# Kernel tuning notes

Measured on AMD Instinct MI355X. Metric: run time of the kernel, lower is better.

## Reference

```python
import jax, jax.numpy as jnp
import numpy as np

B, T, D, H = 8, 4096, 1024, 8
BW = D // H
MIN_DECAY = 0.001
EPS = 1e-05        # RGLRU eps (clamps)
SCAN_EPS = 1e-07   # closed_form_rnn_scan eps


def setup_inputs() -> dict:
    key = jax.random.key(0)
    k0, k1, k2 = jax.random.split(key, 3)
    x = jax.random.normal(k0, (B, T, D), dtype=jnp.float32)
    a_param = jnp.full((D,), -3.0, dtype=jnp.float32)
    # block-diagonal gate params (orthogonal-ish init approximated by scaled normal)
    w_in = jax.random.normal(k1, (H, BW, BW), dtype=jnp.float32) * (1.0 / np.sqrt(BW))
    b_in = jnp.ones((H, BW), dtype=jnp.float32)
    w_a = jax.random.normal(k2, (H, BW, BW), dtype=jnp.float32) * (1.0 / np.sqrt(BW))
    b_a = jnp.ones((H, BW), dtype=jnp.float32)
    return {"x": x, "a_param": a_param, "w_in": w_in, "b_in": b_in, "w_a": w_a, "b_a": b_a}


def block_diag_linear(x, w, b):
    # x: [B,T,D] -> [B,T,H,BW] ; w: [H,BW,BW] ; b: [H,BW]
    xb = x.reshape(x.shape[:-1] + (H, BW))
    y = jnp.einsum('bthi,hij->bthj', xb, w) + b
    return y.reshape(x.shape)


def closed_form_rnn_scan(x, a):
    # x, a: [B,T,D]; h0 = 0
    a_cumprod = jnp.cumprod(a, axis=1)
    ones = jnp.ones((x.shape[0], 1, x.shape[2]), dtype=x.dtype)
    p_prefix = jnp.concatenate([ones, a_cumprod[:, :-1, :]], axis=1)
    p_prefix = jnp.maximum(p_prefix, SCAN_EPS)
    w = (x + SCAN_EPS) / p_prefix
    S = jnp.cumsum(w, axis=1)
    h = p_prefix * S  # + p_prefix * h0 with h0 = 0
    return h, h[:, -1, :]


def reference(x, a_param, w_in, b_in, w_a, b_a):
    gate_x = jax.nn.sigmoid(block_diag_linear(x, w_in, b_in))
    gate_a = jax.nn.sigmoid(block_diag_linear(x, w_a, b_a))
    log_a = -gate_a * (jax.nn.softplus(a_param) + MIN_DECAY)
    a = jnp.minimum(jnp.exp(log_a), 1.0 - EPS)
    gated_x = x * gate_x
    multiplier = jnp.sqrt(jnp.maximum(1.0 - a * a, EPS))
    normed_x = gated_x * multiplier
    h, _ = closed_form_rnn_scan(normed_x, a)
    return h
```

## Files before the change

### kernel.cpp

```cpp
#include <hip/hip_runtime.h>

#define B_ 8
#define T_ 4096
#define D_ 1024
#define H_ 8
#define BW_ 128
#define NC_ 32
#define CT_ 128
#define EPS7 1e-7f
#define EPS5 1e-5f
#define LOG1MEPS -1.0000186e-05f

typedef _Float16 f16x8 __attribute__((ext_vector_type(8)));
typedef _Float16 f16x4 __attribute__((ext_vector_type(4)));
typedef float f32x4 __attribute__((ext_vector_type(4)));

__global__ __launch_bounds__(256) void k1_gates(
    const float* __restrict__ x, const float* __restrict__ a_param,
    const float* __restrict__ w_in, const float* __restrict__ b_in,
    const float* __restrict__ w_a, const float* __restrict__ b_a,
    float* __restrict__ Abuf, float* __restrict__ NX, float* __restrict__ CS)
{
  const int bid  = blockIdx.x;
  const int kc   = bid & (NC_ - 1);
  const int h    = (bid >> 5) & (H_ - 1);
  const int b    = bid >> 8;
  const int tid  = threadIdx.x;
  const int wave = tid >> 6;
  const int lane = tid & 63;
  const int quad = lane >> 4;
  const int l15  = lane & 15;

  __shared__ _Float16 xs[128 * 136];

  const float* xg = x + (size_t)(b * T_ + kc * CT_) * D_ + h * BW_;
  const int jc = wave * 32;

  f16x8 bf[2][2][4];
  #pragma unroll
  for (int g = 0; g < 2; ++g) {
    const float* wptr = (g ? w_a : w_in) + h * BW_ * BW_;
    #pragma unroll
    for (int jt = 0; jt < 2; ++jt) {
      #pragma unroll
      for (int k = 0; k < 4; ++k) {
        const float* wp = wptr + (k * 32 + quad * 8) * BW_ + jc + jt * 16 + l15;
        f16x8 f;
        #pragma unroll
        for (int i = 0; i < 8; ++i) f[i] = (_Float16)wp[i * BW_];
        bf[g][jt][k] = f;
      }
    }
  }
  float bI[2], bA[2], cdec[2];
  #pragma unroll
  for (int jt = 0; jt < 2; ++jt) {
    const int j = h * BW_ + jc + jt * 16 + l15;
    bI[jt] = b_in[j];
    bA[jt] = b_a[j];
    const float ap = a_param[j];
    cdec[jt] = ((ap > 20.f) ? ap : log1pf(__expf(ap))) + 0.001f;
  }

  {
    const int row = tid >> 1;
    const int cb  = (tid & 1) * 64;
    #pragma unroll
    for (int i = 0; i < 16; ++i) {
      const float4 v = *(const float4*)(xg + row * D_ + cb + i * 4);
      f16x4 hv = { (_Float16)v.x, (_Float16)v.y, (_Float16)v.z, (_Float16)v.w };
      *(f16x4*)(xs + row * 136 + cb + i * 4) = hv;
    }
  }
  __syncthreads();

  f32x4 acc[2][2][8];
  #pragma unroll
  for (int g = 0; g < 2; ++g)
    #pragma unroll
    for (int jt = 0; jt < 2; ++jt)
      #pragma unroll
      for (int m = 0; m < 8; ++m)
        acc[g][jt][m] = (f32x4){0.f, 0.f, 0.f, 0.f};

  #pragma unroll
  for (int m = 0; m < 8; ++m) {
    f16x8 af[4];
    #pragma unroll
    for (int k = 0; k < 4; ++k)
      af[k] = *(const f16x8*)(xs + (m * 16 + l15) * 136 + k * 32 + quad * 8);
    #pragma unroll
    for (int k = 0; k < 4; ++k)
      #pragma unroll
      for (int g = 0; g < 2; ++g)
        #pragma unroll
        for (int jt = 0; jt < 2; ++jt)
          acc[g][jt][m] = __builtin_amdgcn_mfma_f32_16x16x32_f16(
              af[k], bf[g][jt][k], acc[g][jt][m], 0, 0, 0);
  }

  float sla[2] = {0.f, 0.f};
  const size_t obase = (size_t)(b * T_ + kc * CT_) * D_ + h * BW_;
  #pragma unroll
  for (int m = 0; m < 8; ++m) {
    #pragma unroll
    for (int r = 0; r < 4; ++r) {
      const int row = m * 16 + quad * 4 + r;
      #pragma unroll
      for (int jt = 0; jt < 2; ++jt) {
        const int col = jc + jt * 16 + l15;
        const float yi = acc[0][jt][m][r] + bI[jt];
        const float ya = acc[1][jt][m][r] + bA[jt];
        const float gx = __builtin_amdgcn_rcpf(1.f + __expf(-yi));
        const float ga = __builtin_amdgcn_rcpf(1.f + __expf(-ya));
        const float la = -ga * cdec[jt];
        const float a  = fminf(__expf(la), 1.0f - EPS5);
        const float mult = sqrtf(fmaxf(fmaf(-a, a, 1.0f), EPS5));
        const float xval = xg[row * D_ + col];
        const float nx = xval * gx * mult;
        const size_t gi = obase + (size_t)row * D_ + col;
        Abuf[gi] = a;
        NX[gi]   = nx;
        sla[jt] += fminf(la, LOG1MEPS);
      }
    }
  }
  #pragma unroll
  for (int jt = 0; jt < 2; ++jt) {
    sla[jt] += __shfl_xor(sla[jt], 16, 64);
    sla[jt] += __shfl_xor(sla[jt], 32, 64);
  }
  if (quad == 0) {
    const int cs = (b * NC_ + kc) * D_ + h * BW_ + jc;
    CS[cs + l15]      = sla[0];
    CS[cs + 16 + l15] = sla[1];
  }
}

__global__ __launch_bounds__(256) void k2_scan_logs(float* __restrict__ CS)
{
  const int idx = blockIdx.x * 256 + threadIdx.x;
  const int b = idx >> 10;
  const int d = idx & (D_ - 1);
  float lq = 0.f;
  #pragma unroll
  for (int kk = 0; kk < NC_; ++kk) {
    const int o = (b * NC_ + kk) * D_ + d;
    const float c = CS[o];
    CS[o] = lq;
    lq += c;
  }
}

__device__ __forceinline__ float scan_r(float c, float pp, float aprev) {
  return (c > EPS7) ? aprev
                    : ((pp > EPS7) ? (EPS7 * __builtin_amdgcn_rcpf(pp)) : 1.0f);
}

__global__ __launch_bounds__(256) void k3_summary(
    const float* __restrict__ Abuf, const float* __restrict__ NX,
    const float* __restrict__ LQ, float* __restrict__ Ak, float* __restrict__ Bk)
{
  const int bid = blockIdx.x;
  const int g = bid & 3;
  const int k = (bid >> 2) & (NC_ - 1);
  const int b = bid >> 7;
  const int d = g * 256 + threadIdx.x;
  const int t0 = k * CT_;
  const size_t base = (size_t)(b * T_ + t0) * D_ + d;

  float c, pp, aprev;
  if (k == 0) { c = 1.f; pp = 1.f; aprev = 1.f; }
  else {
    c = __expf(LQ[(b * NC_ + k) * D_ + d]);
    aprev = Abuf[base - D_];
    pp = fmaxf(c / aprev, EPS7);
  }
  float hv = 0.f, rp = 1.f;
  for (int t = 0; t < CT_; t += 8) {
    float av[8], uv[8];
    #pragma unroll
    for (int i = 0; i < 8; ++i) {
      av[i] = Abuf[base + (size_t)(t + i) * D_];
      uv[i] = NX[base + (size_t)(t + i) * D_] + EPS7;
    }
    #pragma unroll
    for (int i = 0; i < 8; ++i) {
      const float p = fmaxf(c, EPS7);
      const float r = scan_r(c, pp, aprev);
      hv = fmaf(r, hv, uv[i]);
      rp *= r;
      c *= av[i]; pp = p; aprev = av[i];
    }
  }
  Ak[(b * NC_ + k) * D_ + d] = rp;
  Bk[(b * NC_ + k) * D_ + d] = hv;
}

__global__ __launch_bounds__(256) void k3_carry(
    float* __restrict__ Ak, const float* __restrict__ Bk)
{
  const int idx = blockIdx.x * 256 + threadIdx.x;
  const int b = idx >> 10;
  const int d = idx & (D_ - 1);
  float Hv = 0.f;
  #pragma unroll
  for (int kk = 0; kk < NC_; ++kk) {
    const int o = (b * NC_ + kk) * D_ + d;
    const float Av = Ak[o];
    Ak[o] = Hv;
    Hv = fmaf(Av, Hv, Bk[o]);
  }
}

__global__ __launch_bounds__(256) void k3_scan(
    const float* __restrict__ Abuf, float* NXO,
    const float* __restrict__ LQ, const float* __restrict__ Hc)
{
  const int bid = blockIdx.x;
  const int g = bid & 3;
  const int k = (bid >> 2) & (NC_ - 1);
  const int b = bid >> 7;
  const int d = g * 256 + threadIdx.x;
  const int t0 = k * CT_;
  const size_t base = (size_t)(b * T_ + t0) * D_ + d;

  float c, pp, aprev;
  if (k == 0) { c = 1.f; pp = 1.f; aprev = 1.f; }
  else {
    c = __expf(LQ[(b * NC_ + k) * D_ + d]);
    aprev = Abuf[base - D_];
    pp = fmaxf(c / aprev, EPS7);
  }
  float hv = Hc[(b * NC_ + k) * D_ + d];
  for (int t = 0; t < CT_; t += 8) {
    float av[8], uv[8];
    #pragma unroll
    for (int i = 0; i < 8; ++i) {
      av[i] = Abuf[base + (size_t)(t + i) * D_];
      uv[i] = NXO[base + (size_t)(t + i) * D_] + EPS7;
    }
    #pragma unroll
    for (int i = 0; i < 8; ++i) {
      const float p = fmaxf(c, EPS7);
      const float r = scan_r(c, pp, aprev);
      hv = fmaf(r, hv, uv[i]);
      NXO[base + (size_t)(t + i) * D_] = hv;
      c *= av[i]; pp = p; aprev = av[i];
    }
  }
}

extern "C" void kernel_launch(void* const* d_in, const int* in_sizes, int n_in,
                              void* d_out, int out_size, void* d_ws, size_t ws_size,
                              hipStream_t stream) {
  const float* x       = (const float*)d_in[0];
  const float* a_param = (const float*)d_in[1];
  const float* w_in    = (const float*)d_in[2];
  const float* b_in    = (const float*)d_in[3];
  const float* w_a     = (const float*)d_in[4];
  const float* b_a     = (const float*)d_in[5];
  float* out = (float*)d_out;

  char* ws = (char*)d_ws;
  float* Abuf = (float*)ws;
  float* CS   = (float*)(ws + (size_t)B_ * T_ * D_ * 4);
  float* Ak   = CS + B_ * NC_ * D_;
  float* Bk   = Ak + B_ * NC_ * D_;

  k1_gates<<<B_ * H_ * NC_, 256, 0, stream>>>(x, a_param, w_in, b_in, w_a, b_a,
                                              Abuf, out, CS);
  k2_scan_logs<<<(B_ * D_) / 256, 256, 0, stream>>>(CS);
  k3_summary<<<B_ * NC_ * (D_ / 256), 256, 0, stream>>>(Abuf, out, CS, Ak, Bk);
  k3_carry<<<(B_ * D_) / 256, 256, 0, stream>>>(Ak, Bk);
  k3_scan<<<B_ * NC_ * (D_ / 256), 256, 0, stream>>>(Abuf, out, CS, Ak);
}
```

Before: 434.2 us.

## Fuse gate epilogue per MFMA tile and double-buffer scan loads

In the gate kernel, each 16-row MFMA tile's epilogue runs right after its accumulation. This shrinks the live accumulator set from 32 vectors to 4, and x is reread from the fp16 shared-memory copy instead of global memory. In the summary and scan kernels, the next 8 timesteps of A and NX are prefetched while the current 8 are processed, which hides global load latency. Using fp16 x in the gated product adds a small precision loss.

```diff
diff --git a/kernel.cpp b/kernel.cpp
--- a/kernel.cpp
+++ b/kernel.cpp
@@ -74,14 +74,8 @@
   }
   __syncthreads();
 
-  f32x4 acc[2][2][8];
-  #pragma unroll
-  for (int g = 0; g < 2; ++g)
-    #pragma unroll
-    for (int jt = 0; jt < 2; ++jt)
-      #pragma unroll
-      for (int m = 0; m < 8; ++m)
-        acc[g][jt][m] = (f32x4){0.f, 0.f, 0.f, 0.f};
+  float sla[2] = {0.f, 0.f};
+  const size_t obase = (size_t)(b * T_ + kc * CT_) * D_ + h * BW_;
 
   #pragma unroll
   for (int m = 0; m < 8; ++m) {
@@ -89,34 +83,37 @@
     #pragma unroll
     for (int k = 0; k < 4; ++k)
       af[k] = *(const f16x8*)(xs + (m * 16 + l15) * 136 + k * 32 + quad * 8);
+
+    f32x4 acc[2][2];
+    #pragma unroll
+    for (int g = 0; g < 2; ++g)
+      #pragma unroll
+      for (int jt = 0; jt < 2; ++jt)
+        acc[g][jt] = (f32x4){0.f, 0.f, 0.f, 0.f};
+
     #pragma unroll
     for (int k = 0; k < 4; ++k)
       #pragma unroll
       for (int g = 0; g < 2; ++g)
         #pragma unroll
         for (int jt = 0; jt < 2; ++jt)
-          acc[g][jt][m] = __builtin_amdgcn_mfma_f32_16x16x32_f16(
-              af[k], bf[g][jt][k], acc[g][jt][m], 0, 0, 0);
-  }
-
-  float sla[2] = {0.f, 0.f};
-  const size_t obase = (size_t)(b * T_ + kc * CT_) * D_ + h * BW_;
-  #pragma unroll
-  for (int m = 0; m < 8; ++m) {
+          acc[g][jt] = __builtin_amdgcn_mfma_f32_16x16x32_f16(
+              af[k], bf[g][jt][k], acc[g][jt], 0, 0, 0);
+
     #pragma unroll
     for (int r = 0; r < 4; ++r) {
       const int row = m * 16 + quad * 4 + r;
       #pragma unroll
       for (int jt = 0; jt < 2; ++jt) {
         const int col = jc + jt * 16 + l15;
-        const float yi = acc[0][jt][m][r] + bI[jt];
-        const float ya = acc[1][jt][m][r] + bA[jt];
+        const float yi = acc[0][jt][r] + bI[jt];
+        const float ya = acc[1][jt][r] + bA[jt];
         const float gx = __builtin_amdgcn_rcpf(1.f + __expf(-yi));
         const float ga = __builtin_amdgcn_rcpf(1.f + __expf(-ya));
         const float la = -ga * cdec[jt];
         const float a  = fminf(__expf(la), 1.0f - EPS5);
         const float mult = sqrtf(fmaxf(fmaf(-a, a, 1.0f), EPS5));
-        const float xval = xg[row * D_ + col];
+        const float xval = (float)xs[row * 136 + col];
         const float nx = xval * gx * mult;
         const size_t gi = obase + (size_t)row * D_ + col;
         Abuf[gi] = a;
@@ -125,6 +122,7 @@
       }
     }
   }
+
   #pragma unroll
   for (int jt = 0; jt < 2; ++jt) {
     sla[jt] += __shfl_xor(sla[jt], 16, 64);
@@ -169,6 +167,13 @@
   const int t0 = k * CT_;
   const size_t base = (size_t)(b * T_ + t0) * D_ + d;
 
+  float a0[8], u0[8], a1[8], u1[8];
+  #pragma unroll
+  for (int i = 0; i < 8; ++i) {
+    a0[i] = Abuf[base + (size_t)i * D_];
+    u0[i] = NX[base + (size_t)i * D_] + EPS7;
+  }
+
   float c, pp, aprev;
   if (k == 0) { c = 1.f; pp = 1.f; aprev = 1.f; }
   else {
@@ -177,20 +182,37 @@
     pp = fmaxf(c / aprev, EPS7);
   }
   float hv = 0.f, rp = 1.f;
-  for (int t = 0; t < CT_; t += 8) {
-    float av[8], uv[8];
-    #pragma unroll
-    for (int i = 0; i < 8; ++i) {
-      av[i] = Abuf[base + (size_t)(t + i) * D_];
-      uv[i] = NX[base + (size_t)(t + i) * D_] + EPS7;
+
+  #pragma unroll
+  for (int tb = 0; tb < 8; ++tb) {
+    const int tA = tb * 16;
+    #pragma unroll
+    for (int i = 0; i < 8; ++i) {
+      a1[i] = Abuf[base + (size_t)(tA + 8 + i) * D_];
+      u1[i] = NX[base + (size_t)(tA + 8 + i) * D_] + EPS7;
     }
     #pragma unroll
     for (int i = 0; i < 8; ++i) {
       const float p = fmaxf(c, EPS7);
       const float r = scan_r(c, pp, aprev);
-      hv = fmaf(r, hv, uv[i]);
+      hv = fmaf(r, hv, u0[i]);
       rp *= r;
-      c *= av[i]; pp = p; aprev = av[i];
+      c *= a0[i]; pp = p; aprev = a0[i];
+    }
+    if (tb < 7) {
+      #pragma unroll
+      for (int i = 0; i < 8; ++i) {
+        a0[i] = Abuf[base + (size_t)(tA + 16 + i) * D_];
+        u0[i] = NX[base + (size_t)(tA + 16 + i) * D_] + EPS7;
+      }
+    }
+    #pragma unroll
+    for (int i = 0; i < 8; ++i) {
+      const float p = fmaxf(c, EPS7);
+      const float r = scan_r(c, pp, aprev);
+      hv = fmaf(r, hv, u1[i]);
+      rp *= r;
+      c *= a1[i]; pp = p; aprev = a1[i];
     }
   }
   Ak[(b * NC_ + k) * D_ + d] = rp;
@@ -225,6 +247,13 @@
   const int t0 = k * CT_;
   const size_t base = (size_t)(b * T_ + t0) * D_ + d;
 
+  float a0[8], u0[8], a1[8], u1[8];
+  #pragma unroll
+  for (int i = 0; i < 8; ++i) {
+    a0[i] = Abuf[base + (size_t)i * D_];
+    u0[i] = NXO[base + (size_t)i * D_] + EPS7;
+  }
+
   float c, pp, aprev;
   if (k == 0) { c = 1.f; pp = 1.f; aprev = 1.f; }
   else {
@@ -233,20 +262,37 @@
     pp = fmaxf(c / aprev, EPS7);
   }
   float hv = Hc[(b * NC_ + k) * D_ + d];
-  for (int t = 0; t < CT_; t += 8) {
-    float av[8], uv[8];
-    #pragma unroll
-    for (int i = 0; i < 8; ++i) {
-      av[i] = Abuf[base + (size_t)(t + i) * D_];
-      uv[i] = NXO[base + (size_t)(t + i) * D_] + EPS7;
+
+  #pragma unroll
+  for (int tb = 0; tb < 8; ++tb) {
+    const int tA = tb * 16;
+    #pragma unroll
+    for (int i = 0; i < 8; ++i) {
+      a1[i] = Abuf[base + (size_t)(tA + 8 + i) * D_];
+      u1[i] = NXO[base + (size_t)(tA + 8 + i) * D_] + EPS7;
     }
     #pragma unroll
     for (int i = 0; i < 8; ++i) {
       const float p = fmaxf(c, EPS7);
       const float r = scan_r(c, pp, aprev);
-      hv = fmaf(r, hv, uv[i]);
-      NXO[base + (size_t)(t + i) * D_] = hv;
-      c *= av[i]; pp = p; aprev = av[i];
+      hv = fmaf(r, hv, u0[i]);
+      NXO[base + (size_t)(tA + i) * D_] = hv;
+      c *= a0[i]; pp = p; aprev = a0[i];
+    }
+    if (tb < 7) {
+      #pragma unroll
+      for (int i = 0; i < 8; ++i) {
+        a0[i] = Abuf[base + (size_t)(tA + 16 + i) * D_];
+        u0[i] = NXO[base + (size_t)(tA + 16 + i) * D_] + EPS7;
+      }
+    }
+    #pragma unroll
+    for (int i = 0; i < 8; ++i) {
+      const float p = fmaxf(c, EPS7);
+      const float r = scan_r(c, pp, aprev);
+      hv = fmaf(r, hv, u1[i]);
+      NXO[base + (size_t)(tA + 8 + i) * D_] = hv;
+      c *= a1[i]; pp = p; aprev = a1[i];
     }
   }
 }
```

Result: slower. 453.8 us (+4.5%).

## Store intermediate decay and gated input in fp16 and widen scan per-thread work

Applied to the files above, without the earlier changes.

The gate kernel now writes the decay (stored as scaled 1-a) and the normalized input as fp16 instead of fp32, which halves intermediate traffic through the summary and scan passes. It also reads x from the fp16 shared tile instead of global memory. The scan kernels process two channels per thread with half2 loads and double-buffered register prefetch, and write the final output directly. Storing a as fp16 (1-a)*256 loses precision in the decay, which can compound through the products in the scan and risks accuracy failures.

```diff
diff --git a/kernel.cpp b/kernel.cpp
--- a/kernel.cpp
+++ b/kernel.cpp
@@ -7,19 +7,24 @@
 #define BW_ 128
 #define NC_ 32
 #define CT_ 128
+#define DH_ (D_ / 2)
 #define EPS7 1e-7f
 #define EPS5 1e-5f
 #define LOG1MEPS -1.0000186e-05f
+#define OMSCALE 256.0f
+#define INVOMS 0.00390625f
 
 typedef _Float16 f16x8 __attribute__((ext_vector_type(8)));
 typedef _Float16 f16x4 __attribute__((ext_vector_type(4)));
+typedef _Float16 f16x2 __attribute__((ext_vector_type(2)));
 typedef float f32x4 __attribute__((ext_vector_type(4)));
 
 __global__ __launch_bounds__(256) void k1_gates(
     const float* __restrict__ x, const float* __restrict__ a_param,
     const float* __restrict__ w_in, const float* __restrict__ b_in,
     const float* __restrict__ w_a, const float* __restrict__ b_a,
-    float* __restrict__ Abuf, float* __restrict__ NX, float* __restrict__ CS)
+    _Float16* __restrict__ A16, _Float16* __restrict__ NX16,
+    float* __restrict__ CS)
 {
   const int bid  = blockIdx.x;
   const int kc   = bid & (NC_ - 1);
@@ -116,11 +121,11 @@
         const float la = -ga * cdec[jt];
         const float a  = fminf(__expf(la), 1.0f - EPS5);
         const float mult = sqrtf(fmaxf(fmaf(-a, a, 1.0f), EPS5));
-        const float xval = xg[row * D_ + col];
+        const float xval = (float)xs[row * 136 + col];
         const float nx = xval * gx * mult;
         const size_t gi = obase + (size_t)row * D_ + col;
-        Abuf[gi] = a;
-        NX[gi]   = nx;
+        A16[gi]  = (_Float16)((1.0f - a) * OMSCALE);
+        NX16[gi] = (_Float16)nx;
         sla[jt] += fminf(la, LOG1MEPS);
       }
     }
@@ -158,43 +163,72 @@
 }
 
 __global__ __launch_bounds__(256) void k3_summary(
-    const float* __restrict__ Abuf, const float* __restrict__ NX,
+    const _Float16* __restrict__ A16, const _Float16* __restrict__ NX16,
     const float* __restrict__ LQ, float* __restrict__ Ak, float* __restrict__ Bk)
 {
   const int bid = blockIdx.x;
-  const int g = bid & 3;
-  const int k = (bid >> 2) & (NC_ - 1);
-  const int b = bid >> 7;
-  const int d = g * 256 + threadIdx.x;
-  const int t0 = k * CT_;
-  const size_t base = (size_t)(b * T_ + t0) * D_ + d;
-
-  float c, pp, aprev;
-  if (k == 0) { c = 1.f; pp = 1.f; aprev = 1.f; }
+  const int g = bid & 1;
+  const int k = (bid >> 1) & (NC_ - 1);
+  const int b = bid >> 6;
+  const int dp = g * 256 + threadIdx.x;
+  const int d  = dp * 2;
+  const size_t base2 = (size_t)(b * T_ + k * CT_) * DH_ + dp;
+  const f16x2* __restrict__ Av = (const f16x2*)A16;
+  const f16x2* __restrict__ Uv = (const f16x2*)NX16;
+
+  float c0, pp0, ap0, c1, pp1, ap1;
+  if (k == 0) { c0 = c1 = 1.f; pp0 = pp1 = 1.f; ap0 = ap1 = 1.f; }
   else {
-    c = __expf(LQ[(b * NC_ + k) * D_ + d]);
-    aprev = Abuf[base - D_];
-    pp = fmaxf(c / aprev, EPS7);
-  }
-  float hv = 0.f, rp = 1.f;
-  for (int t = 0; t < CT_; t += 8) {
-    float av[8], uv[8];
+    const float2 lq = *(const float2*)&LQ[(b * NC_ + k) * D_ + d];
+    c0 = __expf(lq.x); c1 = __expf(lq.y);
+    const f16x2 ab = Av[base2 - DH_];
+    ap0 = fmaf((float)ab[0], -INVOMS, 1.0f);
+    ap1 = fmaf((float)ab[1], -INVOMS, 1.0f);
+    pp0 = fmaxf(c0 / ap0, EPS7);
+    pp1 = fmaxf(c1 / ap1, EPS7);
+  }
+  float hv0 = 0.f, hv1 = 0.f, rp0 = 1.f, rp1 = 1.f;
+
+  f16x2 bA[2][8], bU[2][8];
+  #pragma unroll
+  for (int i = 0; i < 8; ++i) {
+    bA[0][i] = Av[base2 + (size_t)i * DH_];
+    bU[0][i] = Uv[base2 + (size_t)i * DH_];
+  }
+  #pragma unroll
+  for (int tb = 0; tb < 16; ++tb) {
+    const int cur = tb & 1, nxt = cur ^ 1;
+    if (tb < 15) {
+      const size_t o = base2 + (size_t)((tb + 1) * 8) * DH_;
+      #pragma unroll
+      for (int i = 0; i < 8; ++i) {
+        bA[nxt][i] = Av[o + (size_t)i * DH_];
+        bU[nxt][i] = Uv[o + (size_t)i * DH_];
+      }
+    }
     #pragma unroll
     for (int i = 0; i < 8; ++i) {
-      av[i] = Abuf[base + (size_t)(t + i) * D_];
-      uv[i] = NX[base + (size_t)(t + i) * D_] + EPS7;
-    }
-    #pragma unroll
-    for (int i = 0; i < 8; ++i) {
-      const float p = fmaxf(c, EPS7);
-      const float r = scan_r(c, pp, aprev);
-      hv = fmaf(r, hv, uv[i]);
-      rp *= r;
-      c *= av[i]; pp = p; aprev = av[i];
-    }
-  }
-  Ak[(b * NC_ + k) * D_ + d] = rp;
-  Bk[(b * NC_ + k) * D_ + d] = hv;
+      const float a0 = fmaf((float)bA[cur][i][0], -INVOMS, 1.0f);
+      const float a1 = fmaf((float)bA[cur][i][1], -INVOMS, 1.0f);
+      const float u0 = (float)bU[cur][i][0] + EPS7;
+      const float u1 = (float)bU[cur][i][1] + EPS7;
+      {
+        const float p = fmaxf(c0, EPS7);
+        const float r = scan_r(c0, pp0, ap0);
+        hv0 = fmaf(r, hv0, u0); rp0 *= r;
+        c0 *= a0; pp0 = p; ap0 = a0;
+      }
+      {
+        const float p = fmaxf(c1, EPS7);
+        const float r = scan_r(c1, pp1, ap1);
+        hv1 = fmaf(r, hv1, u1); rp1 *= r;
+        c1 *= a1; pp1 = p; ap1 = a1;
+      }
+    }
+  }
+  const int o = (b * NC_ + k) * D_ + d;
+  *(float2*)&Ak[o] = make_float2(rp0, rp1);
+  *(float2*)&Bk[o] = make_float2(hv0, hv1);
 }
 
 __global__ __launch_bounds__(256) void k3_carry(
@@ -214,39 +248,72 @@
 }
 
 __global__ __launch_bounds__(256) void k3_scan(
-    const float* __restrict__ Abuf, float* NXO,
-    const float* __restrict__ LQ, const float* __restrict__ Hc)
+    const _Float16* __restrict__ A16, const _Float16* __restrict__ NX16,
+    const float* __restrict__ LQ, const float* __restrict__ Hc,
+    float* __restrict__ out)
 {
   const int bid = blockIdx.x;
-  const int g = bid & 3;
-  const int k = (bid >> 2) & (NC_ - 1);
-  const int b = bid >> 7;
-  const int d = g * 256 + threadIdx.x;
-  const int t0 = k * CT_;
-  const size_t base = (size_t)(b * T_ + t0) * D_ + d;
-
-  float c, pp, aprev;
-  if (k == 0) { c = 1.f; pp = 1.f; aprev = 1.f; }
+  const int g = bid & 1;
+  const int k = (bid >> 1) & (NC_ - 1);
+  const int b = bid >> 6;
+  const int dp = g * 256 + threadIdx.x;
+  const int d  = dp * 2;
+  const size_t base2 = (size_t)(b * T_ + k * CT_) * DH_ + dp;
+  const size_t obase = (size_t)(b * T_ + k * CT_) * D_ + d;
+  const f16x2* __restrict__ Av = (const f16x2*)A16;
+  const f16x2* __restrict__ Uv = (const f16x2*)NX16;
+
+  float c0, pp0, ap0, c1, pp1, ap1;
+  if (k == 0) { c0 = c1 = 1.f; pp0 = pp1 = 1.f; ap0 = ap1 = 1.f; }
   else {
-    c = __expf(LQ[(b * NC_ + k) * D_ + d]);
-    aprev = Abuf[base - D_];
-    pp = fmaxf(c / aprev, EPS7);
-  }
-  float hv = Hc[(b * NC_ + k) * D_ + d];
-  for (int t = 0; t < CT_; t += 8) {
-    float av[8], uv[8];
+    const float2 lq = *(const float2*)&LQ[(b * NC_ + k) * D_ + d];
+    c0 = __expf(lq.x); c1 = __expf(lq.y);
+    const f16x2 ab = Av[base2 - DH_];
+    ap0 = fmaf((float)ab[0], -INVOMS, 1.0f);
+    ap1 = fmaf((float)ab[1], -INVOMS, 1.0f);
+    pp0 = fmaxf(c0 / ap0, EPS7);
+    pp1 = fmaxf(c1 / ap1, EPS7);
+  }
+  const float2 hc = *(const float2*)&Hc[(b * NC_ + k) * D_ + d];
+  float hv0 = hc.x, hv1 = hc.y;
+
+  f16x2 bA[2][8], bU[2][8];
+  #pragma unroll
+  for (int i = 0; i < 8; ++i) {
+    bA[0][i] = Av[base2 + (size_t)i * DH_];
+    bU[0][i] = Uv[base2 + (size_t)i * DH_];
+  }
+  #pragma unroll
+  for (int tb = 0; tb < 16; ++tb) {
+    const int cur = tb & 1, nxt = cur ^ 1;
+    if (tb < 15) {
+      const size_t o = base2 + (size_t)((tb + 1) * 8) * DH_;
+      #pragma unroll
+      for (int i = 0; i < 8; ++i) {
+        bA[nxt][i] = Av[o + (size_t)i * DH_];
+        bU[nxt][i] = Uv[o + (size_t)i * DH_];
+      }
+    }
     #pragma unroll
     for (int i = 0; i < 8; ++i) {
-      av[i] = Abuf[base + (size_t)(t + i) * D_];
-      uv[i] = NXO[base + (size_t)(t + i) * D_] + EPS7;
-    }
-    #pragma unroll
-    for (int i = 0; i < 8; ++i) {
-      const float p = fmaxf(c, EPS7);
-      const float r = scan_r(c, pp, aprev);
-      hv = fmaf(r, hv, uv[i]);
-      NXO[base + (size_t)(t + i) * D_] = hv;
-      c *= av[i]; pp = p; aprev = av[i];
+      const int t = tb * 8 + i;
+      const float a0 = fmaf((float)bA[cur][i][0], -INVOMS, 1.0f);
+      const float a1 = fmaf((float)bA[cur][i][1], -INVOMS, 1.0f);
+      const float u0 = (float)bU[cur][i][0] + EPS7;
+      const float u1 = (float)bU[cur][i][1] + EPS7;
+      {
+        const float p = fmaxf(c0, EPS7);
+        const float r = scan_r(c0, pp0, ap0);
+        hv0 = fmaf(r, hv0, u0);
+        c0 *= a0; pp0 = p; ap0 = a0;
+      }
+      {
+        const float p = fmaxf(c1, EPS7);
+        const float r = scan_r(c1, pp1, ap1);
+        hv1 = fmaf(r, hv1, u1);
+        c1 *= a1; pp1 = p; ap1 = a1;
+      }
+      *(float2*)&out[obase + (size_t)t * D_] = make_float2(hv0, hv1);
     }
   }
 }
@@ -263,15 +330,16 @@
   float* out = (float*)d_out;
 
   char* ws = (char*)d_ws;
-  float* Abuf = (float*)ws;
-  float* CS   = (float*)(ws + (size_t)B_ * T_ * D_ * 4);
-  float* Ak   = CS + B_ * NC_ * D_;
-  float* Bk   = Ak + B_ * NC_ * D_;
+  _Float16* A16  = (_Float16*)ws;
+  _Float16* NX16 = (_Float16*)(ws + (size_t)B_ * T_ * D_ * 2);
+  float* CS = (float*)(ws + (size_t)B_ * T_ * D_ * 4);
+  float* Ak = CS + B_ * NC_ * D_;
+  float* Bk = Ak + B_ * NC_ * D_;
 
   k1_gates<<<B_ * H_ * NC_, 256, 0, stream>>>(x, a_param, w_in, b_in, w_a, b_a,
-                                              Abuf, out, CS);
+                                              A16, NX16, CS);
   k2_scan_logs<<<(B_ * D_) / 256, 256, 0, stream>>>(CS);
-  k3_summary<<<B_ * NC_ * (D_ / 256), 256, 0, stream>>>(Abuf, out, CS, Ak, Bk);
+  k3_summary<<<B_ * NC_ * 2, 256, 0, stream>>>(A16, NX16, CS, Ak, Bk);
   k3_carry<<<(B_ * D_) / 256, 256, 0, stream>>>(Ak, Bk);
-  k3_scan<<<B_ * NC_ * (D_ / 256), 256, 0, stream>>>(Abuf, out, CS, Ak);
-}
+  k3_scan<<<B_ * NC_ * 2, 256, 0, stream>>>(A16, NX16, CS, Ak, out);
+}
```

After: 402.8 us. 7.2% less time.

## Pack decay and normalized input as interleaved fp16 pairs for scan passes

Applied to the files above, without the earlier changes.

The gate kernel now stores the decay as a scaled fp16 (1-a)*256 interleaved with the normalized input in fp16, in place of two separate fp32 buffers. It also reuses the fp16 x tile already in shared memory rather than rereading x from global memory. The summary and scan kernels are restructured so each thread handles four channels, using vectorized 16-byte loads with double-buffered prefetch, and the final scan writes to the output directly. This halves the intermediate traffic but costs precision in a and u, which may affect accuracy of the cumulative product.

```diff
diff --git a/kernel.cpp b/kernel.cpp
--- a/kernel.cpp
+++ b/kernel.cpp
@@ -10,16 +10,19 @@
 #define EPS7 1e-7f
 #define EPS5 1e-5f
 #define LOG1MEPS -1.0000186e-05f
+#define OMSCALE 256.0f
+#define INVOMS 0.00390625f
 
 typedef _Float16 f16x8 __attribute__((ext_vector_type(8)));
 typedef _Float16 f16x4 __attribute__((ext_vector_type(4)));
+typedef _Float16 f16x2 __attribute__((ext_vector_type(2)));
 typedef float f32x4 __attribute__((ext_vector_type(4)));
 
 __global__ __launch_bounds__(256) void k1_gates(
     const float* __restrict__ x, const float* __restrict__ a_param,
     const float* __restrict__ w_in, const float* __restrict__ b_in,
     const float* __restrict__ w_a, const float* __restrict__ b_a,
-    float* __restrict__ Abuf, float* __restrict__ NX, float* __restrict__ CS)
+    f16x2* __restrict__ AU, float* __restrict__ CS)
 {
   const int bid  = blockIdx.x;
   const int kc   = bid & (NC_ - 1);
@@ -34,7 +37,7 @@
   __shared__ _Float16 xs[128 * 136];
 
   const float* xg = x + (size_t)(b * T_ + kc * CT_) * D_ + h * BW_;
-  const int jc = wave * 32;
+  const int jcp = wave * 32 + 2 * l15;
 
   f16x8 bf[2][2][4];
   #pragma unroll
@@ -44,7 +47,7 @@
     for (int jt = 0; jt < 2; ++jt) {
       #pragma unroll
       for (int k = 0; k < 4; ++k) {
-        const float* wp = wptr + (k * 32 + quad * 8) * BW_ + jc + jt * 16 + l15;
+        const float* wp = wptr + (k * 32 + quad * 8) * BW_ + jcp + jt;
         f16x8 f;
         #pragma unroll
         for (int i = 0; i < 8; ++i) f[i] = (_Float16)wp[i * BW_];
@@ -55,7 +58,7 @@
   float bI[2], bA[2], cdec[2];
   #pragma unroll
   for (int jt = 0; jt < 2; ++jt) {
-    const int j = h * BW_ + jc + jt * 16 + l15;
+    const int j = h * BW_ + jcp + jt;
     bI[jt] = b_in[j];
     bA[jt] = b_a[j];
     const float ap = a_param[j];
@@ -63,13 +66,14 @@
   }
 
   {
-    const int row = tid >> 1;
-    const int cb  = (tid & 1) * 64;
+    const int rr = tid >> 5;
+    const int cc = (tid & 31) * 4;
     #pragma unroll
     for (int i = 0; i < 16; ++i) {
-      const float4 v = *(const float4*)(xg + row * D_ + cb + i * 4);
+      const int row = i * 8 + rr;
+      const float4 v = *(const float4*)(xg + row * D_ + cc);
       f16x4 hv = { (_Float16)v.x, (_Float16)v.y, (_Float16)v.z, (_Float16)v.w };
-      *(f16x4*)(xs + row * 136 + cb + i * 4) = hv;
+      *(f16x4*)(xs + row * 136 + cc) = hv;
     }
   }
   __syncthreads();
@@ -100,15 +104,16 @@
   }
 
   float sla[2] = {0.f, 0.f};
-  const size_t obase = (size_t)(b * T_ + kc * CT_) * D_ + h * BW_;
+  const size_t obase = (size_t)(b * T_ + kc * CT_) * D_ + h * BW_ + jcp;
   #pragma unroll
   for (int m = 0; m < 8; ++m) {
     #pragma unroll
     for (int r = 0; r < 4; ++r) {
       const int row = m * 16 + quad * 4 + r;
+      const f16x2 xv = *(const f16x2*)(xs + row * 136 + jcp);
+      float aenc[2], nxv[2];
       #pragma unroll
       for (int jt = 0; jt < 2; ++jt) {
-        const int col = jc + jt * 16 + l15;
         const float yi = acc[0][jt][m][r] + bI[jt];
         const float ya = acc[1][jt][m][r] + bA[jt];
         const float gx = __builtin_amdgcn_rcpf(1.f + __expf(-yi));
@@ -116,13 +121,13 @@
         const float la = -ga * cdec[jt];
         const float a  = fminf(__expf(la), 1.0f - EPS5);
         const float mult = sqrtf(fmaxf(fmaf(-a, a, 1.0f), EPS5));
-        const float xval = xg[row * D_ + col];
-        const float nx = xval * gx * mult;
-        const size_t gi = obase + (size_t)row * D_ + col;
-        Abuf[gi] = a;
-        NX[gi]   = nx;
+        aenc[jt] = (1.0f - a) * OMSCALE;
+        nxv[jt]  = (float)xv[jt] * gx * mult;
         sla[jt] += fminf(la, LOG1MEPS);
       }
+      f16x4 st = { (_Float16)aenc[0], (_Float16)nxv[0],
+                   (_Float16)aenc[1], (_Float16)nxv[1] };
+      *(f16x4*)&AU[obase + (size_t)row * D_] = st;
     }
   }
   #pragma unroll
@@ -131,9 +136,8 @@
     sla[jt] += __shfl_xor(sla[jt], 32, 64);
   }
   if (quad == 0) {
-    const int cs = (b * NC_ + kc) * D_ + h * BW_ + jc;
-    CS[cs + l15]      = sla[0];
-    CS[cs + 16 + l15] = sla[1];
+    const int csb = (b * NC_ + kc) * D_ + h * BW_ + jcp;
+    *(float2*)&CS[csb] = make_float2(sla[0], sla[1]);
   }
 }
 
@@ -158,43 +162,64 @@
 }
 
 __global__ __launch_bounds__(256) void k3_summary(
-    const float* __restrict__ Abuf, const float* __restrict__ NX,
-    const float* __restrict__ LQ, float* __restrict__ Ak, float* __restrict__ Bk)
-{
-  const int bid = blockIdx.x;
-  const int g = bid & 3;
-  const int k = (bid >> 2) & (NC_ - 1);
-  const int b = bid >> 7;
-  const int d = g * 256 + threadIdx.x;
-  const int t0 = k * CT_;
-  const size_t base = (size_t)(b * T_ + t0) * D_ + d;
-
-  float c, pp, aprev;
-  if (k == 0) { c = 1.f; pp = 1.f; aprev = 1.f; }
-  else {
-    c = __expf(LQ[(b * NC_ + k) * D_ + d]);
-    aprev = Abuf[base - D_];
-    pp = fmaxf(c / aprev, EPS7);
-  }
-  float hv = 0.f, rp = 1.f;
-  for (int t = 0; t < CT_; t += 8) {
-    float av[8], uv[8];
+    const f16x2* __restrict__ AU, const float* __restrict__ LQ,
+    float* __restrict__ Ak, float* __restrict__ Bk)
+{
+  const int k = blockIdx.x & (NC_ - 1);
+  const int b = blockIdx.x >> 5;
+  const int d0 = threadIdx.x * 4;
+  const size_t base = (size_t)(b * T_ + k * CT_) * D_ + d0;
+
+  float c[4], pp[4], ap[4], hv[4], rp[4];
+  if (k == 0) {
+    #pragma unroll
+    for (int ch = 0; ch < 4; ++ch) { c[ch] = 1.f; pp[ch] = 1.f; ap[ch] = 1.f; }
+  } else {
+    const float4 lq = *(const float4*)&LQ[(b * NC_ + k) * D_ + d0];
+    const f16x8 ab = *(const f16x8*)&AU[base - D_];
+    const float lqa[4] = {lq.x, lq.y, lq.z, lq.w};
+    #pragma unroll
+    for (int ch = 0; ch < 4; ++ch) {
+      c[ch]  = __expf(lqa[ch]);
+      ap[ch] = fmaf((float)ab[2 * ch], -INVOMS, 1.0f);
+      pp[ch] = fmaxf(c[ch] / ap[ch], EPS7);
+    }
+  }
+  #pragma unroll
+  for (int ch = 0; ch < 4; ++ch) { hv[ch] = 0.f; rp[ch] = 1.f; }
+
+  f16x8 buf[2][8];
+  #pragma unroll
+  for (int i = 0; i < 8; ++i)
+    buf[0][i] = *(const f16x8*)&AU[base + (size_t)i * D_];
+
+  #pragma unroll
+  for (int tb = 0; tb < 16; ++tb) {
+    const int cur = tb & 1, nxt = cur ^ 1;
+    if (tb < 15) {
+      const size_t o = base + (size_t)((tb + 1) * 8) * D_;
+      #pragma unroll
+      for (int i = 0; i < 8; ++i)
+        buf[nxt][i] = *(const f16x8*)&AU[o + (size_t)i * D_];
+    }
     #pragma unroll
     for (int i = 0; i < 8; ++i) {
-      av[i] = Abuf[base + (size_t)(t + i) * D_];
-      uv[i] = NX[base + (size_t)(t + i) * D_] + EPS7;
-    }
-    #pragma unroll
-    for (int i = 0; i < 8; ++i) {
-      const float p = fmaxf(c, EPS7);
-      const float r = scan_r(c, pp, aprev);
-      hv = fmaf(r, hv, uv[i]);
-      rp *= r;
-      c *= av[i]; pp = p; aprev = av[i];
-    }
-  }
-  Ak[(b * NC_ + k) * D_ + d] = rp;
-  Bk[(b * NC_ + k) * D_ + d] = hv;
+      const f16x8 f = buf[cur][i];
+      #pragma unroll
+      for (int ch = 0; ch < 4; ++ch) {
+        const float a = fmaf((float)f[2 * ch], -INVOMS, 1.0f);
+        const float u = (float)f[2 * ch + 1] + EPS7;
+        const float p = fmaxf(c[ch], EPS7);
+        const float r = scan_r(c[ch], pp[ch], ap[ch]);
+        hv[ch] = fmaf(r, hv[ch], u);
+        rp[ch] *= r;
+        c[ch] *= a; pp[ch] = p; ap[ch] = a;
+      }
+    }
+  }
+  const int o = (b * NC_ + k) * D_ + d0;
+  *(float4*)&Ak[o] = (float4){rp[0], rp[1], rp[2], rp[3]};
+  *(float4*)&Bk[o] = (float4){hv[0], hv[1], hv[2], hv[3]};
 }
 
 __global__ __launch_bounds__(256) void k3_carry(
@@ -214,39 +239,63 @@
 }
 
 __global__ __launch_bounds__(256) void k3_scan(
-    const float* __restrict__ Abuf, float* NXO,
-    const float* __restrict__ LQ, const float* __restrict__ Hc)
-{
-  const int bid = blockIdx.x;
-  const int g = bid & 3;
-  const int k = (bid >> 2) & (NC_ - 1);
-  const int b = bid >> 7;
-  const int d = g * 256 + threadIdx.x;
-  const int t0 = k * CT_;
-  const size_t base = (size_t)(b * T_ + t0) * D_ + d;
-
-  float c, pp, aprev;
-  if (k == 0) { c = 1.f; pp = 1.f; aprev = 1.f; }
-  else {
-    c = __expf(LQ[(b * NC_ + k) * D_ + d]);
-    aprev = Abuf[base - D_];
-    pp = fmaxf(c / aprev, EPS7);
-  }
-  float hv = Hc[(b * NC_ + k) * D_ + d];
-  for (int t = 0; t < CT_; t += 8) {
-    float av[8], uv[8];
+    const f16x2* __restrict__ AU, const float* __restrict__ LQ,
+    const float* __restrict__ Hc, float* __restrict__ out)
+{
+  const int k = blockIdx.x & (NC_ - 1);
+  const int b = blockIdx.x >> 5;
+  const int d0 = threadIdx.x * 4;
+  const size_t base = (size_t)(b * T_ + k * CT_) * D_ + d0;
+  float* __restrict__ op = out + base;
+
+  float c[4], pp[4], ap[4], hv[4];
+  if (k == 0) {
+    #pragma unroll
+    for (int ch = 0; ch < 4; ++ch) { c[ch] = 1.f; pp[ch] = 1.f; ap[ch] = 1.f; }
+  } else {
+    const float4 lq = *(const float4*)&LQ[(b * NC_ + k) * D_ + d0];
+    const f16x8 ab = *(const f16x8*)&AU[base - D_];
+    const float lqa[4] = {lq.x, lq.y, lq.z, lq.w};
+    #pragma unroll
+    for (int ch = 0; ch < 4; ++ch) {
+      c[ch]  = __expf(lqa[ch]);
+      ap[ch] = fmaf((float)ab[2 * ch], -INVOMS, 1.0f);
+      pp[ch] = fmaxf(c[ch] / ap[ch], EPS7);
+    }
+  }
+  {
+    const float4 hc = *(const float4*)&Hc[(b * NC_ + k) * D_ + d0];
+    hv[0] = hc.x; hv[1] = hc.y; hv[2] = hc.z; hv[3] = hc.w;
+  }
+
+  f16x8 buf[2][8];
+  #pragma unroll
+  for (int i = 0; i < 8; ++i)
+    buf[0][i] = *(const f16x8*)&AU[base + (size_t)i * D_];
+
+  #pragma unroll
+  for (int tb = 0; tb < 16; ++tb) {
+    const int cur = tb & 1, nxt = cur ^ 1;
+    if (tb < 15) {
+      const size_t o = base + (size_t)((tb + 1) * 8) * D_;
+      #pragma unroll
+      for (int i = 0; i < 8; ++i)
+        buf[nxt][i] = *(const f16x8*)&AU[o + (size_t)i * D_];
+    }
     #pragma unroll
     for (int i = 0; i < 8; ++i) {
-      av[i] = Abuf[base + (size_t)(t + i) * D_];
-      uv[i] = NXO[base + (size_t)(t + i) * D_] + EPS7;
-    }
-    #pragma unroll
-    for (int i = 0; i < 8; ++i) {
-      const float p = fmaxf(c, EPS7);
-      const float r = scan_r(c, pp, aprev);
-      hv = fmaf(r, hv, uv[i]);
-      NXO[base + (size_t)(t + i) * D_] = hv;
-      c *= av[i]; pp = p; aprev = av[i];
+      const f16x8 f = buf[cur][i];
+      #pragma unroll
+      for (int ch = 0; ch < 4; ++ch) {
+        const float a = fmaf((float)f[2 * ch], -INVOMS, 1.0f);
+        const float u = (float)f[2 * ch + 1] + EPS7;
+        const float p = fmaxf(c[ch], EPS7);
+        const float r = scan_r(c[ch], pp[ch], ap[ch]);
+        hv[ch] = fmaf(r, hv[ch], u);
+        c[ch] *= a; pp[ch] = p; ap[ch] = a;
+      }
+      *(float4*)&op[(size_t)(tb * 8 + i) * D_] =
+          (float4){hv[0], hv[1], hv[2], hv[3]};
     }
   }
 }
@@ -263,15 +312,15 @@
   float* out = (float*)d_out;
 
   char* ws = (char*)d_ws;
-  float* Abuf = (float*)ws;
-  float* CS   = (float*)(ws + (size_t)B_ * T_ * D_ * 4);
-  float* Ak   = CS + B_ * NC_ * D_;
-  float* Bk   = Ak + B_ * NC_ * D_;
+  f16x2* AU = (f16x2*)ws;
+  float* CS = (float*)(ws + (size_t)B_ * T_ * D_ * 4);
+  float* Ak = CS + B_ * NC_ * D_;
+  float* Bk = Ak + B_ * NC_ * D_;
 
   k1_gates<<<B_ * H_ * NC_, 256, 0, stream>>>(x, a_param, w_in, b_in, w_a, b_a,
-                                              Abuf, out, CS);
+                                              AU, CS);
   k2_scan_logs<<<(B_ * D_) / 256, 256, 0, stream>>>(CS);
-  k3_summary<<<B_ * NC_ * (D_ / 256), 256, 0, stream>>>(Abuf, out, CS, Ak, Bk);
+  k3_summary<<<B_ * NC_, 256, 0, stream>>>(AU, CS, Ak, Bk);
   k3_carry<<<(B_ * D_) / 256, 256, 0, stream>>>(Ak, Bk);
-  k3_scan<<<B_ * NC_ * (D_ / 256), 256, 0, stream>>>(Abuf, out, CS, Ak);
-}
+  k3_scan<<<B_ * NC_, 256, 0, stream>>>(AU, CS, Ak, out);
+}
```

Result: slower. 498.1 us (+14.7%).
